# Performance work log

Measured on AMD Instinct MI355X. Metric: run time of the kernel, lower is better.

Reference implementation:

```python
import jax, jax.numpy as jnp
import numpy as np

T, B = 384, 128
IN_DIM, HID, OUT_DIM = 512, 1024, 512


def _lstm_step(h, c, x_t, Wx, Wh, b):
    # x_t: [B, D], h/c: [B, H]; gates order: i, f, g, o
    gates = x_t @ Wx + h @ Wh + b  # [B, 4H]
    i, f, g, o = jnp.split(gates, 4, axis=-1)
    c_new = jax.nn.sigmoid(f) * c + jax.nn.sigmoid(i) * jnp.tanh(g)
    h_new = jax.nn.sigmoid(o) * jnp.tanh(c_new)
    return h_new, c_new


def setup_inputs() -> dict:
    key = jax.random.key(0)
    ks = jax.random.split(key, 9)
    s_in = 1.0 / np.sqrt(IN_DIM)
    s_h = 1.0 / np.sqrt(HID)
    s_o = 1.0 / np.sqrt(OUT_DIM)
    return {
        "x": jax.random.normal(ks[0], (T, B, IN_DIM), dtype=jnp.float32),
        "hidden_state": jnp.zeros((1, B, HID), dtype=jnp.float32),
        "cell_state": jnp.zeros((1, B, HID), dtype=jnp.float32),
        "enc_Wx": jax.random.normal(ks[1], (IN_DIM, 4 * HID), dtype=jnp.float32) * s_in,
        "enc_Wh": jax.random.normal(ks[2], (HID, 4 * HID), dtype=jnp.float32) * s_h,
        "enc_b": jnp.zeros((4 * HID,), dtype=jnp.float32),
        "dec_Wx": jax.random.normal(ks[3], (OUT_DIM, 4 * HID), dtype=jnp.float32) * s_o,
        "dec_Wh": jax.random.normal(ks[4], (HID, 4 * HID), dtype=jnp.float32) * s_h,
        "dec_b": jnp.zeros((4 * HID,), dtype=jnp.float32),
        "fc_W": jax.random.normal(ks[5], (HID, OUT_DIM), dtype=jnp.float32) * s_h,
        "fc_b": jnp.zeros((OUT_DIM,), dtype=jnp.float32),
    }


def reference(x, hidden_state, cell_state, enc_Wx, enc_Wh, enc_b,
              dec_Wx, dec_Wh, dec_b, fc_W, fc_b):
    # ---- encoder: run LSTM over T steps, keep only final hidden state ----
    h0, c0 = hidden_state[0], cell_state[0]  # [B, H]

    def enc_step(carry, x_t):
        h, c = carry
        h, c = _lstm_step(h, c, x_t, enc_Wx, enc_Wh, enc_b)
        return (h, c), None

    (h_enc, _), _ = jax.lax.scan(enc_step, (h0, c0), x)

    y0 = jnp.zeros((B, OUT_DIM), dtype=x.dtype)
    c_dec0 = jnp.zeros((B, HID), dtype=x.dtype)

    def dec_step(carry, _):
        y, h, c = carry
        h, c = _lstm_step(h, c, y, dec_Wx, dec_Wh, dec_b)
        y = jax.nn.softmax(h @ fc_W + fc_b, axis=-1)  # softmax over dim=2
        return (y, h, c), y

    _, output = jax.lax.scan(dec_step, (y0, h_enc, c_dec0), None, length=T)
    return output  # [T, B, OUT_DIM]
```

## Files before the change

kernel.cpp:

```cpp
#include <hip/hip_runtime.h>


#define TS 384

typedef __attribute__((ext_vector_type(8))) short bf16x8;
typedef __attribute__((ext_vector_type(4))) float f32x4;

#define WS_XR 4096u
#define XR_SLOT 262144u
#define WS_HP (WS_XR + 4u*XR_SLOT)
#define HP_BUF 524288u
#define WS_FPN (WS_HP + 2u*HP_BUF)
#define WS_TOTAL (WS_FPN + 2097152u)

#define MFMA __builtin_amdgcn_mfma_f32_16x16x32_bf16

__device__ __forceinline__ unsigned short bf16r(float v) {
  unsigned u = __float_as_uint(v);
  u += 0x7FFFu + ((u >> 16) & 1u);
  return (unsigned short)(u >> 16);
}
__device__ __forceinline__ float bf2f(unsigned short h) {
  return __uint_as_float(((unsigned)h) << 16);
}
__device__ __forceinline__ void split2(float v, short& hi, short& lo) {
  unsigned short h = bf16r(v);
  float r = v - bf2f(h);
  hi = (short)h; lo = (short)bf16r(r);
}
__device__ __forceinline__ float sigm(float v)  { return 1.0f / (1.0f + __expf(-v)); }
__device__ __forceinline__ float tanhfa(float v){ return 1.0f - 2.0f / (__expf(2.0f*v) + 1.0f); }

__device__ __forceinline__ void st_u64(void* p, unsigned long long v) {
  __hip_atomic_store((unsigned long long*)p, v, __ATOMIC_RELAXED, __HIP_MEMORY_SCOPE_AGENT);
}
__device__ __forceinline__ unsigned long long ld_u64(const void* p) {
  return __hip_atomic_load((const unsigned long long*)p, __ATOMIC_RELAXED, __HIP_MEMORY_SCOPE_AGENT);
}
__device__ __forceinline__ void st_u32(unsigned* p, unsigned v) {
  __hip_atomic_store(p, v, __ATOMIC_RELAXED, __HIP_MEMORY_SCOPE_AGENT);
}
__device__ __forceinline__ unsigned ld_u32(const unsigned* p) {
  return __hip_atomic_load(p, __ATOMIC_RELAXED, __HIP_MEMORY_SCOPE_AGENT);
}
__device__ __forceinline__ void st_f32(float* p, float v) {
  __hip_atomic_store(p, v, __ATOMIC_RELAXED, __HIP_MEMORY_SCOPE_AGENT);
}
__device__ __forceinline__ float ld_f32(const float* p) {
  return __hip_atomic_load(p, __ATOMIC_RELAXED, __HIP_MEMORY_SCOPE_AGENT);
}

__device__ __forceinline__ void setflag(unsigned* flag, unsigned val) {
  asm volatile("s_waitcnt vmcnt(0)" ::: "memory");
  __syncthreads();
  if (threadIdx.x == 0)
    __hip_atomic_store(flag, val, __ATOMIC_RELAXED, __HIP_MEMORY_SCOPE_AGENT);
}
__device__ __forceinline__ void hwait(const unsigned* flags, unsigned* invdone_line,
                                      bool leader, unsigned target, int* sDead) {
  if (leader) {
    if (threadIdx.x < 64) {
      const unsigned long long* q = (const unsigned long long*)(flags + threadIdx.x * 4);
      unsigned spins = 0;
      for (;;) {
        unsigned long long q0 = ld_u64(q), q1 = ld_u64(q + 1);
        bool ok = ((unsigned)q0 >= target) && ((unsigned)(q0 >> 32) >= target)
               && ((unsigned)q1 >= target) && ((unsigned)(q1 >> 32) >= target);
        if (__all(ok)) break;
        if (++spins > (1u << 20)) { if (threadIdx.x == 0) *sDead = 1; break; }
      }
    }
    if (threadIdx.x == 0) {
      __builtin_amdgcn_fence(__ATOMIC_ACQUIRE, "agent");
      st_u32(invdone_line, target);
      asm volatile("s_waitcnt vmcnt(0)" ::: "memory");
    }
  } else {
    if (threadIdx.x == 0) {
      unsigned spins = 0;
      while (ld_u32(invdone_line) < target) {
        if (++spins > (1u << 20)) { *sDead = 1; break; }
      }
      asm volatile("buffer_inv sc0" ::: "memory");
      asm volatile("s_waitcnt vmcnt(0)" ::: "memory");
    }
  }
  __syncthreads();
}
__device__ __forceinline__ void wait128(const unsigned* flags, unsigned target, int* sDead) {
  if (threadIdx.x < 64) {
    const int i = threadIdx.x;
    const bool act = (i * 4) < 128;
    const unsigned long long* q = (const unsigned long long*)(flags + i * 4);
    unsigned spins = 0;
    for (;;) {
      bool ok = true;
      if (act) {
        unsigned long long q0 = ld_u64(q), q1 = ld_u64(q + 1);
        ok = ((unsigned)q0 >= target) && ((unsigned)(q0 >> 32) >= target)
          && ((unsigned)q1 >= target) && ((unsigned)(q1 >> 32) >= target);
      }
      if (__all(ok)) break;
      if (++spins > (1u << 20)) { if (i == 0) *sDead = 1; break; }
    }
  }
  __syncthreads();
}

__device__ void load_gate_weights(const float* __restrict__ Wx, const float* __restrict__ Wh,
                                  int p, short* sBh, short* sBl) {
  for (int idx = threadIdx.x; idx < 24576; idx += 1024) {
    int j = idx & 7, l = (idx >> 3) & 63, kb = idx >> 9;
    int k = kb * 32 + ((l >> 4) << 3) + j;
    int c = l & 15;
    int gcol = (c >> 2) * 1024 + p * 4 + (c & 3);
    float wv = (k < 512) ? Wx[(size_t)k * 4096 + gcol]
                         : Wh[(size_t)(k - 512) * 4096 + gcol];
    short hi, lo; split2(wv, hi, lo);
    sBh[idx] = hi; sBl[idx] = lo;
  }
}
__device__ void load_fc_weights(const float* __restrict__ fcW, int kg, int cg,
                                short* sFh, short* sFl) {
  for (int idx = threadIdx.x; idx < 4096; idx += 1024) {
    int j = idx & 7, l = (idx >> 3) & 63, kb = idx >> 9;
    int unit = kg * 256 + kb * 32 + ((l >> 4) << 3) + j;
    int col = cg * 16 + (l & 15);
    short hi, lo; split2(fcW[(size_t)unit * 512 + col], hi, lo);
    sFh[idx] = hi; sFl[idx] = lo;
  }
}

template<int NKB, int D>
__device__ __forceinline__ void gg_pipe(const short* AH_, const short* AL_,
    const short* BH_, const short* BL_, int mt, int l,
    int kbA0, int kbB0, f32x4* acc)
{
  const bf16x8* AH = (const bf16x8*)AH_;
  const bf16x8* AL = (const bf16x8*)AL_;
  const bf16x8* BH = (const bf16x8*)BH_;
  const bf16x8* BL = (const bf16x8*)BL_;
  bf16x8 pah[D], pal[D];
  #pragma unroll
  for (int i = 0; i < D; ++i) {
    pah[i] = AH[((kbA0 + i) * 8 + mt) * 64 + l];
    pal[i] = AL[((kbA0 + i) * 8 + mt) * 64 + l];
  }
  #pragma unroll
  for (int i = 0; i < NKB; ++i) {
    bf16x8 ah = pah[i % D], al = pal[i % D];
    if (i + D < NKB) {
      pah[i % D] = AH[((kbA0 + i + D) * 8 + mt) * 64 + l];
      pal[i % D] = AL[((kbA0 + i + D) * 8 + mt) * 64 + l];
    }
    bf16x8 bh = BH[(kbB0 + i) * 64 + l];
    bf16x8 bl = BL[(kbB0 + i) * 64 + l];
    const int a = (i & 1) * 3;
    acc[a + 0] = MFMA(ah, bh, acc[a + 0], 0, 0, 0);
    acc[a + 1] = MFMA(ah, bl, acc[a + 1], 0, 0, 0);
    acc[a + 2] = MFMA(al, bh, acc[a + 2], 0, 0, 0);
  }
}
__device__ __forceinline__ void gg_finish(f32x4* acc, int kh, int mt, int l,
                                          float* LDSgate) {
  f32x4 s = (acc[0] + acc[3]) + ((acc[1] + acc[4]) + (acc[2] + acc[5]));
  const int col = l & 15, r0 = mt * 16 + ((l >> 4) << 2);
  float* plane = LDSgate + kh * 2176;
  #pragma unroll
  for (int j = 0; j < 4; ++j) plane[(r0 + j) * 17 + col] = s[j];
}

__device__ __forceinline__ void conv_x(const float* __restrict__ xsrc,
                                       short* dstH, short* dstL, int p, int tl) {
  if (tl < 32) {
    int g = p * 32 + tl;
    int l = g & 63, mt = (g >> 6) & 7, kb = g >> 9;
    int row = mt * 16 + (l & 15), k = kb * 32 + ((l >> 4) << 3);
    const float* xs = xsrc + (size_t)row * 512 + k;
    unsigned long long h64[2] = {0, 0}, l64[2] = {0, 0};
    #pragma unroll
    for (int j = 0; j < 8; ++j) {
      short hi, lo; split2(xs[j], hi, lo);
      h64[j >> 2] |= (unsigned long long)(unsigned short)hi << ((j & 3) * 16);
      l64[j >> 2] |= (unsigned long long)(unsigned short)lo << ((j & 3) * 16);
    }
    int off = g * 8;
    st_u64(dstH + off, h64[0]); st_u64(dstH + off + 4, h64[1]);
    st_u64(dstL + off, l64[0]); st_u64(dstL + off + 4, l64[1]);
  }
}

__global__ void __launch_bounds__(1024, 1)
lstm12(const float* __restrict__ x, const float* __restrict__ h0p,
       const float* __restrict__ c0p, const float* __restrict__ eWx,
       const float* __restrict__ eWh, const float* __restrict__ eb,
       const float* __restrict__ dWx, const float* __restrict__ dWh,
       const float* __restrict__ db, const float* __restrict__ fcW,
       const float* __restrict__ fcb, float* __restrict__ out,
       char* __restrict__ ws)
{
  __shared__ __align__(16) short sBh[24576], sBl[24576];
  __shared__ __align__(16) short sFh[4096], sFl[4096];
  __shared__ float LDSgate[2 * 2176];
  __shared__ unsigned hsplit[512];
  __shared__ float ybuf[512];
  __shared__ float red[16];
  __shared__ int sDead, sLeader, sXcd;

  const int p = blockIdx.x, t = threadIdx.x;
  const int w = t >> 6, l = t & 63;
  const int mt = w & 7, kh = w >> 3;
  if (t == 0) sDead = 0;

  unsigned* hflag = (unsigned*)ws;
  unsigned* yflag = (unsigned*)(ws + 1024);
  unsigned* fflag = (unsigned*)(ws + 2048);
  unsigned* elect = (unsigned*)(ws + 3264);

  if (t == 0) {
    unsigned xcd;
    asm volatile("s_getreg_b32 %0, hwreg(HW_REG_XCC_ID)" : "=s"(xcd));
    xcd &= 7u;
    sXcd = (int)xcd;
    unsigned old = __hip_atomic_fetch_add(&elect[xcd], 1u, __ATOMIC_ACQ_REL,
                                          __HIP_MEMORY_SCOPE_AGENT);
    sLeader = (old == 0u) ? 1 : 0;
  }
  __syncthreads();
  const bool leader = (sLeader != 0);
  unsigned* invd = (unsigned*)(ws + 3328 + sXcd * 64);

  short* xrH[4]; short* xrL[4];
  #pragma unroll
  for (int s4 = 0; s4 < 4; ++s4) {
    xrH[s4] = (short*)(ws + WS_XR + s4 * XR_SLOT);
    xrL[s4] = (short*)(ws + WS_XR + s4 * XR_SLOT + 131072u);
  }
  short* hpH[2]; short* hpL[2];
  #pragma unroll
  for (int b2 = 0; b2 < 2; ++b2) {
    hpH[b2] = (short*)(ws + WS_HP + b2 * HP_BUF);
    hpL[b2] = (short*)(ws + WS_HP + b2 * HP_BUF + 262144u);
  }
  float* fp = (float*)(ws + WS_FPN);

  const int row_pw = t & 127, u_pw = (t >> 7) & 3;

  load_gate_weights(eWx, eWh, p, sBh, sBl);
  conv_x(x, xrH[0], xrL[0], p, t);
  conv_x(x + 65536, xrH[1], xrL[1], p, t);
  if (t < 64) {
    int hg = p * 64 + t;
    int ll = hg & 63, mtt = (hg >> 6) & 7, hk = hg >> 9;
    int row = mtt * 16 + (ll & 15), k = hk * 32 + ((ll >> 4) << 3);
    const float* hs = h0p + (size_t)row * 1024 + k;
    unsigned long long h64[2] = {0, 0}, l64[2] = {0, 0};
    #pragma unroll
    for (int j = 0; j < 8; ++j) {
      short hi, lo; split2(hs[j], hi, lo);
      h64[j >> 2] |= (unsigned long long)(unsigned short)hi << ((j & 3) * 16);
      l64[j >> 2] |= (unsigned long long)(unsigned short)lo << ((j & 3) * 16);
    }
    int off = hg * 8;
    st_u64(hpH[0] + off, h64[0]); st_u64(hpH[0] + off + 4, h64[1]);
    st_u64(hpL[0] + off, l64[0]); st_u64(hpL[0] + off + 4, l64[1]);
  }
  float creg = 0.f, bq0 = 0.f, bq1 = 0.f, bq2 = 0.f, bq3 = 0.f;
  if (t < 512) {
    creg = c0p[(size_t)row_pw * 1024 + p * 4 + u_pw];
    bq0 = eb[0 * 1024 + p * 4 + u_pw];
    bq1 = eb[1 * 1024 + p * 4 + u_pw];
    bq2 = eb[2 * 1024 + p * 4 + u_pw];
    bq3 = eb[3 * 1024 + p * 4 + u_pw];
  }
  setflag(&hflag[p], 1u);
  hwait(hflag, invd, leader, 1u, &sDead);
  if (sDead) return;

  for (int st = 0; st < TS; ++st) {
    int rb = st & 1, wb = rb ^ 1, xs = st & 3;
    f32x4 z = {0.f, 0.f, 0.f, 0.f};
    f32x4 acc[6] = {z, z, z, z, z, z};
    gg_pipe<8, 4>(xrH[xs], xrL[xs], sBh, sBl, mt, l, kh * 8, kh * 8, acc);
    hwait(hflag, invd, leader, (unsigned)(st + 1), &sDead);
    if (sDead) return;
    gg_pipe<16, 4>(hpH[rb], hpL[rb], sBh, sBl, mt, l, kh * 16, 16 + kh * 16, acc);
    gg_finish(acc, kh, mt, l, LDSgate);
    __syncthreads();
    if (t < 512) {
      float g0 = LDSgate[row_pw * 17 + 0  + u_pw] + LDSgate[2176 + row_pw * 17 + 0  + u_pw] + bq0;
      float g1 = LDSgate[row_pw * 17 + 4  + u_pw] + LDSgate[2176 + row_pw * 17 + 4  + u_pw] + bq1;
      float g2 = LDSgate[row_pw * 17 + 8  + u_pw] + LDSgate[2176 + row_pw * 17 + 8  + u_pw] + bq2;
      float g3 = LDSgate[row_pw * 17 + 12 + u_pw] + LDSgate[2176 + row_pw * 17 + 12 + u_pw] + bq3;
      creg = sigm(g1) * creg + sigm(g0) * tanhfa(g2);
      float h = sigm(g3) * tanhfa(creg);
      short hi, lo; split2(h, hi, lo);
      hsplit[u_pw * 128 + row_pw] = ((unsigned)(unsigned short)hi << 16) | (unsigned short)lo;
    } else if (st + 2 < TS) {
      conv_x(x + (size_t)(st + 2) * 65536, xrH[(st + 2) & 3], xrL[(st + 2) & 3], p, t - 512);
    }
    __syncthreads();
    if (t < 128) {
      int r = t;
      unsigned w0 = hsplit[r], w1 = hsplit[128 + r], w2 = hsplit[256 + r], w3 = hsplit[384 + r];
      unsigned long long hi64 = (unsigned long long)(w0 >> 16)
        | ((unsigned long long)(w1 >> 16) << 16)
        | ((unsigned long long)(w2 >> 16) << 32)
        | ((unsigned long long)(w3 >> 16) << 48);
      unsigned long long lo64 = (unsigned long long)(w0 & 0xFFFFu)
        | ((unsigned long long)(w1 & 0xFFFFu) << 16)
        | ((unsigned long long)(w2 & 0xFFFFu) << 32)
        | ((unsigned long long)(w3 & 0xFFFFu) << 48);
      int hk = p >> 3, mtt = r >> 4;
      int lane_ = (((p >> 1) & 3) << 4) | (r & 15);
      int off = ((hk * 8 + mtt) * 64 + lane_) * 8 + (p & 1) * 4;
      st_u64(hpH[wb] + off, hi64);
      st_u64(hpL[wb] + off, lo64);
    }
    setflag(&hflag[p], (unsigned)(st + 2));
  }

  load_gate_weights(dWx, dWh, p, sBh, sBl);
  if (p >= 128) load_fc_weights(fcW, (p - 128) >> 5, (p - 128) & 31, sFh, sFl);
  if (t < 32) {
    int off = (p * 32 + t) * 8;
    st_u64(xrH[0] + off, 0ull); st_u64(xrH[0] + off + 4, 0ull);
    st_u64(xrL[0] + off, 0ull); st_u64(xrL[0] + off + 4, 0ull);
  }
  creg = 0.0f;
  if (t < 512) {
    bq0 = db[0 * 1024 + p * 4 + u_pw];
    bq1 = db[1 * 1024 + p * 4 + u_pw];
    bq2 = db[2 * 1024 + p * 4 + u_pw];
    bq3 = db[3 * 1024 + p * 4 + u_pw];
  }
  float fcb_r = (t < 512) ? fcb[t] : 0.f;
  setflag(&hflag[p], (unsigned)(TS + 2));

  const unsigned DB = (unsigned)(TS + 2);
  for (int st = 0; st < TS; ++st) {
    const int rb = st & 1, wb = rb ^ 1;
    f32x4 z = {0.f, 0.f, 0.f, 0.f};
    f32x4 acc[6] = {z, z, z, z, z, z};
    hwait(hflag, invd, leader, DB + (unsigned)st, &sDead);
    if (sDead) return;
    if (p >= 128) {
      const int f = p - 128, kg = f >> 5, cg = f & 31;
      if (st >= 1) {
        const bf16x8* AH = (const bf16x8*)hpH[rb];
        const bf16x8* AL = (const bf16x8*)hpL[rb];
        const bf16x8* FB = (const bf16x8*)sFh;
        const bf16x8* FL = (const bf16x8*)sFl;
        f32x4 a0 = z, a1 = z, a2 = z;
        #pragma unroll
        for (int kb = 0; kb < 4; ++kb) {
          int gkb = kg * 8 + kh * 4 + kb;
          bf16x8 ah = AH[(gkb * 8 + mt) * 64 + l];
          bf16x8 al = AL[(gkb * 8 + mt) * 64 + l];
          bf16x8 bh = FB[(kh * 4 + kb) * 64 + l];
          bf16x8 bl = FL[(kh * 4 + kb) * 64 + l];
          a0 = MFMA(ah, bh, a0, 0, 0, 0);
          a1 = MFMA(ah, bl, a1, 0, 0, 0);
          a2 = MFMA(al, bh, a2, 0, 0, 0);
        }
        f32x4 s = a0 + (a1 + a2);
        int slice = kg * 2 + kh;
        int col = cg * 16 + (l & 15), r0 = mt * 16 + ((l >> 4) << 2);
        #pragma unroll
        for (int j = 0; j < 4; ++j)
          st_f32(&fp[(size_t)(slice * 128 + r0 + j) * 512 + col], s[j]);
        setflag(&fflag[f], (unsigned)st);
      }
      gg_pipe<16, 4>(hpH[rb], hpL[rb], sBh, sBl, mt, l, kh * 16, 16 + kh * 16, acc);
      if (st >= 1) { wait128(yflag, (unsigned)st, &sDead); if (sDead) return; }
      gg_pipe<8, 4>(xrH[rb], xrL[rb], sBh, sBl, mt, l, kh * 8, kh * 8, acc);
    } else {
      gg_pipe<16, 4>(hpH[rb], hpL[rb], sBh, sBl, mt, l, kh * 16, 16 + kh * 16, acc);
      if (st >= 1) {
        wait128(fflag, (unsigned)st, &sDead);
        if (sDead) return;
        float v = 0.f, e = 0.f, mx;
        if (t < 512) {
          float tv[8];
          #pragma unroll
          for (int s8 = 0; s8 < 8; ++s8)
            tv[s8] = ld_f32(&fp[(size_t)(s8 * 128 + p) * 512 + t]);
          v = fcb_r + ((tv[0] + tv[1]) + (tv[2] + tv[3]))
                    + ((tv[4] + tv[5]) + (tv[6] + tv[7]));
          mx = v;
          #pragma unroll
          for (int o = 32; o > 0; o >>= 1) mx = fmaxf(mx, __shfl_xor(mx, o));
          if (l == 0) red[w] = mx;
        }
        __syncthreads();
        if (t < 512) {
          mx = red[0];
          #pragma unroll
          for (int i = 1; i < 8; ++i) mx = fmaxf(mx, red[i]);
          e = __expf(v - mx);
          float ss = e;
          #pragma unroll
          for (int o = 32; o > 0; o >>= 1) ss += __shfl_xor(ss, o);
          if (l == 0) red[8 + w] = ss;
        }
        __syncthreads();
        if (t < 512) {
          float ss = (red[8] + red[9]) + (red[10] + red[11])
                   + (red[12] + red[13]) + (red[14] + red[15]);
          float y = e / ss;
          st_f32(&out[((size_t)(st - 1) * 128 + p) * 512 + t], y);
          ybuf[t] = y;
        }
        __syncthreads();
        if (t < 64) {
          int kb = t >> 2, seg = t & 3;
          int k = kb * 32 + seg * 8;
          int lane_ = (seg << 4) | (p & 15), mtt = p >> 4;
          int off = ((kb * 8 + mtt) * 64 + lane_) * 8;
          unsigned long long h64[2] = {0, 0}, l64[2] = {0, 0};
          #pragma unroll
          for (int j = 0; j < 8; ++j) {
            short hi, lo; split2(ybuf[k + j], hi, lo);
            h64[j >> 2] |= (unsigned long long)(unsigned short)hi << ((j & 3) * 16);
            l64[j >> 2] |= (unsigned long long)(unsigned short)lo << ((j & 3) * 16);
          }
          st_u64(xrH[rb] + off, h64[0]); st_u64(xrH[rb] + off + 4, h64[1]);
          st_u64(xrL[rb] + off, l64[0]); st_u64(xrL[rb] + off + 4, l64[1]);
        }
        setflag(&yflag[p], (unsigned)st);
        wait128(yflag, (unsigned)st, &sDead);
        if (sDead) return;
      }
      gg_pipe<8, 4>(xrH[rb], xrL[rb], sBh, sBl, mt, l, kh * 8, kh * 8, acc);
    }
    gg_finish(acc, kh, mt, l, LDSgate);
    __syncthreads();
    if (t < 512) {
      float g0 = LDSgate[row_pw * 17 + 0  + u_pw] + LDSgate[2176 + row_pw * 17 + 0  + u_pw] + bq0;
      float g1 = LDSgate[row_pw * 17 + 4  + u_pw] + LDSgate[2176 + row_pw * 17 + 4  + u_pw] + bq1;
      float g2 = LDSgate[row_pw * 17 + 8  + u_pw] + LDSgate[2176 + row_pw * 17 + 8  + u_pw] + bq2;
      float g3 = LDSgate[row_pw * 17 + 12 + u_pw] + LDSgate[2176 + row_pw * 17 + 12 + u_pw] + bq3;
      creg = sigm(g1) * creg + sigm(g0) * tanhfa(g2);
      float h = sigm(g3) * tanhfa(creg);
      short hi, lo; split2(h, hi, lo);
      hsplit[u_pw * 128 + row_pw] = ((unsigned)(unsigned short)hi << 16) | (unsigned short)lo;
    }
    __syncthreads();
    if (t < 128) {
      int r = t;
      unsigned w0 = hsplit[r], w1 = hsplit[128 + r], w2 = hsplit[256 + r], w3 = hsplit[384 + r];
      unsigned long long hi64 = (unsigned long long)(w0 >> 16)
        | ((unsigned long long)(w1 >> 16) << 16)
        | ((unsigned long long)(w2 >> 16) << 32)
        | ((unsigned long long)(w3 >> 16) << 48);
      unsigned long long lo64 = (unsigned long long)(w0 & 0xFFFFu)
        | ((unsigned long long)(w1 & 0xFFFFu) << 16)
        | ((unsigned long long)(w2 & 0xFFFFu) << 32)
        | ((unsigned long long)(w3 & 0xFFFFu) << 48);
      int hk = p >> 3, mtt = r >> 4;
      int lane_ = (((p >> 1) & 3) << 4) | (r & 15);
      int off = ((hk * 8 + mtt) * 64 + lane_) * 8 + (p & 1) * 4;
      st_u64(hpH[wb] + off, hi64);
      st_u64(hpL[wb] + off, lo64);
    }
    setflag(&hflag[p], DB + (unsigned)(st + 1));
  }

  {
    const int rb = TS & 1;
    hwait(hflag, invd, leader, DB + (unsigned)TS, &sDead);
    if (sDead) return;
    if (p >= 128) {
      const int f = p - 128, kg = f >> 5, cg = f & 31;
      const bf16x8* AH = (const bf16x8*)hpH[rb];
      const bf16x8* AL = (const bf16x8*)hpL[rb];
      const bf16x8* FB = (const bf16x8*)sFh;
      const bf16x8* FL = (const bf16x8*)sFl;
      f32x4 z = {0.f, 0.f, 0.f, 0.f};
      f32x4 a0 = z, a1 = z, a2 = z;
      #pragma unroll
      for (int kb = 0; kb < 4; ++kb) {
        int gkb = kg * 8 + kh * 4 + kb;
        bf16x8 ah = AH[(gkb * 8 + mt) * 64 + l];
        bf16x8 al = AL[(gkb * 8 + mt) * 64 + l];
        bf16x8 bh = FB[(kh * 4 + kb) * 64 + l];
        bf16x8 bl = FL[(kh * 4 + kb) * 64 + l];
        a0 = MFMA(ah, bh, a0, 0, 0, 0);
        a1 = MFMA(ah, bl, a1, 0, 0, 0);
        a2 = MFMA(al, bh, a2, 0, 0, 0);
      }
      f32x4 s = a0 + (a1 + a2);
      int slice = kg * 2 + kh;
      int col = cg * 16 + (l & 15), r0 = mt * 16 + ((l >> 4) << 2);
      #pragma unroll
      for (int j = 0; j < 4; ++j)
        st_f32(&fp[(size_t)(slice * 128 + r0 + j) * 512 + col], s[j]);
      setflag(&fflag[f], (unsigned)TS);
    } else {
      wait128(fflag, (unsigned)TS, &sDead);
      if (sDead) return;
      float v = 0.f, e = 0.f, mx;
      if (t < 512) {
        float tv[8];
        #pragma unroll
        for (int s8 = 0; s8 < 8; ++s8)
          tv[s8] = ld_f32(&fp[(size_t)(s8 * 128 + p) * 512 + t]);
        v = fcb_r + ((tv[0] + tv[1]) + (tv[2] + tv[3]))
                  + ((tv[4] + tv[5]) + (tv[6] + tv[7]));
        mx = v;
        #pragma unroll
        for (int o = 32; o > 0; o >>= 1) mx = fmaxf(mx, __shfl_xor(mx, o));
        if (l == 0) red[w] = mx;
      }
      __syncthreads();
      if (t < 512) {
        mx = red[0];
        #pragma unroll
        for (int i = 1; i < 8; ++i) mx = fmaxf(mx, red[i]);
        e = __expf(v - mx);
        float ss = e;
        #pragma unroll
        for (int o = 32; o > 0; o >>= 1) ss += __shfl_xor(ss, o);
        if (l == 0) red[8 + w] = ss;
      }
      __syncthreads();
      if (t < 512) {
        float ss = (red[8] + red[9]) + (red[10] + red[11])
                 + (red[12] + red[13]) + (red[14] + red[15]);
        st_f32(&out[((size_t)(TS - 1) * 128 + p) * 512 + t], e / ss);
      }
    }
  }
}

extern "C" void kernel_launch(void* const* d_in, const int* in_sizes, int n_in,
                              void* d_out, int out_size, void* d_ws, size_t ws_size,
                              hipStream_t stream) {
  const float* x   = (const float*)d_in[0];
  const float* h0  = (const float*)d_in[1];
  const float* c0  = (const float*)d_in[2];
  const float* eWx = (const float*)d_in[3];
  const float* eWh = (const float*)d_in[4];
  const float* eb  = (const float*)d_in[5];
  const float* dWx = (const float*)d_in[6];
  const float* dWh = (const float*)d_in[7];
  const float* db  = (const float*)d_in[8];
  const float* fcW = (const float*)d_in[9];
  const float* fcb = (const float*)d_in[10];
  float* out = (float*)d_out;

  if (ws_size < (size_t)WS_TOTAL) {
    hipMemsetAsync(d_out, 0xFF, (size_t)out_size * sizeof(float), stream);
    return;
  }
  hipMemsetAsync(d_ws, 0, 4096, stream);
  hipLaunchKernelGGL(lstm12, dim3(256), dim3(1024), 0, stream,
                     x, h0, c0, eWx, eWh, eb, dWx, dWh, db, fcW, fcb, out,
                     (char*)d_ws);
}
```

Measured before the change: 13.74 ms.

## Use cached stores for h/x staging with a cross-XCD writeback barrier

```diff
diff --git a/kernel.cpp b/kernel.cpp
--- a/kernel.cpp
+++ b/kernel.cpp
@@ -31,23 +31,26 @@
 __device__ __forceinline__ float sigm(float v)  { return 1.0f / (1.0f + __expf(-v)); }
 __device__ __forceinline__ float tanhfa(float v){ return 1.0f - 2.0f / (__expf(2.0f*v) + 1.0f); }
 
-__device__ __forceinline__ void st_u64(void* p, unsigned long long v) {
+__device__ __forceinline__ void st_u64_uc(void* p, unsigned long long v) {
   __hip_atomic_store((unsigned long long*)p, v, __ATOMIC_RELAXED, __HIP_MEMORY_SCOPE_AGENT);
 }
-__device__ __forceinline__ unsigned long long ld_u64(const void* p) {
+__device__ __forceinline__ unsigned long long ld_u64_uc(const void* p) {
   return __hip_atomic_load((const unsigned long long*)p, __ATOMIC_RELAXED, __HIP_MEMORY_SCOPE_AGENT);
 }
-__device__ __forceinline__ void st_u32(unsigned* p, unsigned v) {
+__device__ __forceinline__ void st_u32_uc(unsigned* p, unsigned v) {
   __hip_atomic_store(p, v, __ATOMIC_RELAXED, __HIP_MEMORY_SCOPE_AGENT);
 }
-__device__ __forceinline__ unsigned ld_u32(const unsigned* p) {
+__device__ __forceinline__ unsigned ld_u32_uc(const unsigned* p) {
   return __hip_atomic_load(p, __ATOMIC_RELAXED, __HIP_MEMORY_SCOPE_AGENT);
 }
-__device__ __forceinline__ void st_f32(float* p, float v) {
+__device__ __forceinline__ void st_f32_uc(float* p, float v) {
   __hip_atomic_store(p, v, __ATOMIC_RELAXED, __HIP_MEMORY_SCOPE_AGENT);
 }
-__device__ __forceinline__ float ld_f32(const float* p) {
+__device__ __forceinline__ float ld_f32_uc(const float* p) {
   return __hip_atomic_load(p, __ATOMIC_RELAXED, __HIP_MEMORY_SCOPE_AGENT);
+}
+__device__ __forceinline__ void st_u64_c(void* p, unsigned long long v) {
+  *(volatile unsigned long long*)p = v;
 }
 
 __device__ __forceinline__ void setflag(unsigned* flag, unsigned val) {
@@ -56,14 +59,15 @@
   if (threadIdx.x == 0)
     __hip_atomic_store(flag, val, __ATOMIC_RELAXED, __HIP_MEMORY_SCOPE_AGENT);
 }
-__device__ __forceinline__ void hwait(const unsigned* flags, unsigned* invdone_line,
-                                      bool leader, unsigned target, int* sDead) {
+__device__ __forceinline__ void hwait(const unsigned* flags, unsigned* wbdone,
+                                      unsigned* invdone_line, bool leader,
+                                      unsigned target, int* sDead) {
   if (leader) {
     if (threadIdx.x < 64) {
       const unsigned long long* q = (const unsigned long long*)(flags + threadIdx.x * 4);
       unsigned spins = 0;
       for (;;) {
-        unsigned long long q0 = ld_u64(q), q1 = ld_u64(q + 1);
+        unsigned long long q0 = ld_u64_uc(q), q1 = ld_u64_uc(q + 1);
         bool ok = ((unsigned)q0 >= target) && ((unsigned)(q0 >> 32) >= target)
                && ((unsigned)q1 >= target) && ((unsigned)(q1 >> 32) >= target);
         if (__all(ok)) break;
@@ -71,41 +75,17 @@
       }
     }
     if (threadIdx.x == 0) {
-      __builtin_amdgcn_fence(__ATOMIC_ACQUIRE, "agent");
-      st_u32(invdone_line, target);
+      __builtin_amdgcn_fence(__ATOMIC_RELEASE, "agent");
       asm volatile("s_waitcnt vmcnt(0)" ::: "memory");
-    }
-  } else {
-    if (threadIdx.x == 0) {
-      unsigned spins = 0;
-      while (ld_u32(invdone_line) < target) {
-        if (++spins > (1u << 20)) { *sDead = 1; break; }
-      }
-      asm volatile("buffer_inv sc0" ::: "memory");
-      asm volatile("s_waitcnt vmcnt(0)" ::: "memory");
+      st_u32_uc(wbdone + (int)( ((size_t)invdone_line >> 6) & 7 ), 0);
     }
   }
   __syncthreads();
-}
-__device__ __forceinline__ void wait128(const unsigned* flags, unsigned target, int* sDead) {
-  if (threadIdx.x < 64) {
-    const int i = threadIdx.x;
-    const bool act = (i * 4) < 128;
-    const unsigned long long* q = (const unsigned long long*)(flags + i * 4);
-    unsigned spins = 0;
-    for (;;) {
-      bool ok = true;
-      if (act) {
-        unsigned long long q0 = ld_u64(q), q1 = ld_u64(q + 1);
-        ok = ((unsigned)q0 >= target) && ((unsigned)(q0 >> 32) >= target)
-          && ((unsigned)q1 >= target) && ((unsigned)(q1 >> 32) >= target);
-      }
-      if (__all(ok)) break;
-      if (++spins > (1u << 20)) { if (i == 0) *sDead = 1; break; }
-    }
-  }
-  __syncthreads();
-}
+  (void)wbdone;
+  (void)invdone_line;
+  (void)sDead;
+}
+
 
 __device__ void load_gate_weights(const float* __restrict__ Wx, const float* __restrict__ Wh,
                                   int p, short* sBh, short* sBl) {
@@ -185,13 +165,13 @@
       l64[j >> 2] |= (unsigned long long)(unsigned short)lo << ((j & 3) * 16);
     }
     int off = g * 8;
-    st_u64(dstH + off, h64[0]); st_u64(dstH + off + 4, h64[1]);
-    st_u64(dstL + off, l64[0]); st_u64(dstL + off + 4, l64[1]);
+    st_u64_c(dstH + off, h64[0]); st_u64_c(dstH + off + 4, h64[1]);
+    st_u64_c(dstL + off, l64[0]); st_u64_c(dstL + off + 4, l64[1]);
   }
 }
 
 __global__ void __launch_bounds__(1024, 1)
-lstm12(const float* __restrict__ x, const float* __restrict__ h0p,
+lstm13(const float* __restrict__ x, const float* __restrict__ h0p,
        const float* __restrict__ c0p, const float* __restrict__ eWx,
        const float* __restrict__ eWh, const float* __restrict__ eb,
        const float* __restrict__ dWx, const float* __restrict__ dWh,
@@ -212,10 +192,11 @@
   const int mt = w & 7, kh = w >> 3;
   if (t == 0) sDead = 0;
 
-  unsigned* hflag = (unsigned*)ws;
-  unsigned* yflag = (unsigned*)(ws + 1024);
-  unsigned* fflag = (unsigned*)(ws + 2048);
-  unsigned* elect = (unsigned*)(ws + 3264);
+  unsigned* hflag  = (unsigned*)ws;
+  unsigned* yflag  = (unsigned*)(ws + 1024);
+  unsigned* fflag  = (unsigned*)(ws + 2048);
+  unsigned* elect  = (unsigned*)(ws + 3264);
+  unsigned* wbdone = (unsigned*)(ws + 3904);
 
   if (t == 0) {
     unsigned xcd;
@@ -228,7 +209,71 @@
   }
   __syncthreads();
   const bool leader = (sLeader != 0);
-  unsigned* invd = (unsigned*)(ws + 3328 + sXcd * 64);
+  const int myxcd = sXcd;
+  unsigned* invd = (unsigned*)(ws + 3328 + myxcd * 64);
+
+  auto HWAIT = [&](unsigned target) {
+    if (leader) {
+      if (t < 64) {
+        const unsigned long long* q = (const unsigned long long*)(hflag + t * 4);
+        unsigned spins = 0;
+        for (;;) {
+          unsigned long long q0 = ld_u64_uc(q), q1 = ld_u64_uc(q + 1);
+          bool ok = ((unsigned)q0 >= target) && ((unsigned)(q0 >> 32) >= target)
+                 && ((unsigned)q1 >= target) && ((unsigned)(q1 >> 32) >= target);
+          if (__all(ok)) break;
+          if (++spins > (1u << 20)) { if (t == 0) sDead = 1; break; }
+        }
+      }
+      if (t == 0) {
+        __builtin_amdgcn_fence(__ATOMIC_RELEASE, "agent");
+        asm volatile("s_waitcnt vmcnt(0)" ::: "memory");
+        st_u32_uc(&wbdone[myxcd], target);
+        unsigned spins = 0;
+        for (;;) {
+          unsigned long long a = ld_u64_uc(wbdone), b = ld_u64_uc(wbdone + 2);
+          unsigned long long c = ld_u64_uc(wbdone + 4), d = ld_u64_uc(wbdone + 6);
+          bool ok = ((unsigned)a >= target) && ((unsigned)(a >> 32) >= target)
+                 && ((unsigned)b >= target) && ((unsigned)(b >> 32) >= target)
+                 && ((unsigned)c >= target) && ((unsigned)(c >> 32) >= target)
+                 && ((unsigned)d >= target) && ((unsigned)(d >> 32) >= target);
+          if (ok) break;
+          if (++spins > (1u << 20)) { sDead = 1; break; }
+        }
+        __builtin_amdgcn_fence(__ATOMIC_ACQUIRE, "agent");
+        st_u32_uc(invd, target);
+        asm volatile("s_waitcnt vmcnt(0)" ::: "memory");
+      }
+    } else {
+      if (t == 0) {
+        unsigned spins = 0;
+        while (ld_u32_uc(invd) < target) {
+          if (++spins > (1u << 20)) { sDead = 1; break; }
+        }
+        asm volatile("buffer_inv sc0" ::: "memory");
+        asm volatile("s_waitcnt vmcnt(0)" ::: "memory");
+      }
+    }
+    __syncthreads();
+  };
+  auto WAIT128 = [&](const unsigned* flags, unsigned target) {
+    if (t < 64) {
+      const bool act = (t * 4) < 128;
+      const unsigned long long* q = (const unsigned long long*)(flags + t * 4);
+      unsigned spins = 0;
+      for (;;) {
+        bool ok = true;
+        if (act) {
+          unsigned long long q0 = ld_u64_uc(q), q1 = ld_u64_uc(q + 1);
+          ok = ((unsigned)q0 >= target) && ((unsigned)(q0 >> 32) >= target)
+            && ((unsigned)q1 >= target) && ((unsigned)(q1 >> 32) >= target);
+        }
+        if (__all(ok)) break;
+        if (++spins > (1u << 20)) { if (t == 0) sDead = 1; break; }
+      }
+    }
+    __syncthreads();
+  };
 
   short* xrH[4]; short* xrL[4];
   #pragma unroll
@@ -262,8 +307,8 @@
       l64[j >> 2] |= (unsigned long long)(unsigned short)lo << ((j & 3) * 16);
     }
     int off = hg * 8;
-    st_u64(hpH[0] + off, h64[0]); st_u64(hpH[0] + off + 4, h64[1]);
-    st_u64(hpL[0] + off, l64[0]); st_u64(hpL[0] + off + 4, l64[1]);
+    st_u64_c(hpH[0] + off, h64[0]); st_u64_c(hpH[0] + off + 4, h64[1]);
+    st_u64_c(hpL[0] + off, l64[0]); st_u64_c(hpL[0] + off + 4, l64[1]);
   }
   float creg = 0.f, bq0 = 0.f, bq1 = 0.f, bq2 = 0.f, bq3 = 0.f;
   if (t < 512) {
@@ -274,7 +319,7 @@
     bq3 = eb[3 * 1024 + p * 4 + u_pw];
   }
   setflag(&hflag[p], 1u);
-  hwait(hflag, invd, leader, 1u, &sDead);
+  HWAIT(1u);
   if (sDead) return;
 
   for (int st = 0; st < TS; ++st) {
@@ -282,7 +327,7 @@
     f32x4 z = {0.f, 0.f, 0.f, 0.f};
     f32x4 acc[6] = {z, z, z, z, z, z};
     gg_pipe<8, 4>(xrH[xs], xrL[xs], sBh, sBl, mt, l, kh * 8, kh * 8, acc);
-    hwait(hflag, invd, leader, (unsigned)(st + 1), &sDead);
+    HWAIT((unsigned)(st + 1));
     if (sDead) return;
     gg_pipe<16, 4>(hpH[rb], hpL[rb], sBh, sBl, mt, l, kh * 16, 16 + kh * 16, acc);
     gg_finish(acc, kh, mt, l, LDSgate);
@@ -314,8 +359,8 @@
       int hk = p >> 3, mtt = r >> 4;
       int lane_ = (((p >> 1) & 3) << 4) | (r & 15);
       int off = ((hk * 8 + mtt) * 64 + lane_) * 8 + (p & 1) * 4;
-      st_u64(hpH[wb] + off, hi64);
-      st_u64(hpL[wb] + off, lo64);
+      st_u64_c(hpH[wb] + off, hi64);
+      st_u64_c(hpL[wb] + off, lo64);
     }
     setflag(&hflag[p], (unsigned)(st + 2));
   }
@@ -324,8 +369,8 @@
   if (p >= 128) load_fc_weights(fcW, (p - 128) >> 5, (p - 128) & 31, sFh, sFl);
   if (t < 32) {
     int off = (p * 32 + t) * 8;
-    st_u64(xrH[0] + off, 0ull); st_u64(xrH[0] + off + 4, 0ull);
-    st_u64(xrL[0] + off, 0ull); st_u64(xrL[0] + off + 4, 0ull);
+    st_u64_c(xrH[0] + off, 0ull); st_u64_c(xrH[0] + off + 4, 0ull);
+    st_u64_c(xrL[0] + off, 0ull); st_u64_c(xrL[0] + off + 4, 0ull);
   }
   creg = 0.0f;
   if (t < 512) {
@@ -342,7 +387,7 @@
     const int rb = st & 1, wb = rb ^ 1;
     f32x4 z = {0.f, 0.f, 0.f, 0.f};
     f32x4 acc[6] = {z, z, z, z, z, z};
-    hwait(hflag, invd, leader, DB + (unsigned)st, &sDead);
+    HWAIT(DB + (unsigned)st);
     if (sDead) return;
     if (p >= 128) {
       const int f = p - 128, kg = f >> 5, cg = f & 31;
@@ -368,23 +413,23 @@
         int col = cg * 16 + (l & 15), r0 = mt * 16 + ((l >> 4) << 2);
         #pragma unroll
         for (int j = 0; j < 4; ++j)
-          st_f32(&fp[(size_t)(slice * 128 + r0 + j) * 512 + col], s[j]);
+          st_f32_uc(&fp[(size_t)(slice * 128 + r0 + j) * 512 + col], s[j]);
         setflag(&fflag[f], (unsigned)st);
       }
       gg_pipe<16, 4>(hpH[rb], hpL[rb], sBh, sBl, mt, l, kh * 16, 16 + kh * 16, acc);
-      if (st >= 1) { wait128(yflag, (unsigned)st, &sDead); if (sDead) return; }
+      if (st >= 1) { WAIT128(yflag, (unsigned)st); if (sDead) return; }
       gg_pipe<8, 4>(xrH[rb], xrL[rb], sBh, sBl, mt, l, kh * 8, kh * 8, acc);
     } else {
       gg_pipe<16, 4>(hpH[rb], hpL[rb], sBh, sBl, mt, l, kh * 16, 16 + kh * 16, acc);
       if (st >= 1) {
-        wait128(fflag, (unsigned)st, &sDead);
+        WAIT128(fflag, (unsigned)st);
         if (sDead) return;
         float v = 0.f, e = 0.f, mx;
         if (t < 512) {
           float tv[8];
           #pragma unroll
           for (int s8 = 0; s8 < 8; ++s8)
-            tv[s8] = ld_f32(&fp[(size_t)(s8 * 128 + p) * 512 + t]);
+            tv[s8] = ld_f32_uc(&fp[(size_t)(s8 * 128 + p) * 512 + t]);
           v = fcb_r + ((tv[0] + tv[1]) + (tv[2] + tv[3]))
                     + ((tv[4] + tv[5]) + (tv[6] + tv[7]));
           mx = v;
@@ -408,7 +453,7 @@
           float ss = (red[8] + red[9]) + (red[10] + red[11])
                    + (red[12] + red[13]) + (red[14] + red[15]);
           float y = e / ss;
-          st_f32(&out[((size_t)(st - 1) * 128 + p) * 512 + t], y);
+          st_f32_uc(&out[((size_t)(st - 1) * 128 + p) * 512 + t], y);
           ybuf[t] = y;
         }
         __syncthreads();
@@ -424,11 +469,11 @@
             h64[j >> 2] |= (unsigned long long)(unsigned short)hi << ((j & 3) * 16);
             l64[j >> 2] |= (unsigned long long)(unsigned short)lo << ((j & 3) * 16);
           }
-          st_u64(xrH[rb] + off, h64[0]); st_u64(xrH[rb] + off + 4, h64[1]);
-          st_u64(xrL[rb] + off, l64[0]); st_u64(xrL[rb] + off + 4, l64[1]);
+          st_u64_uc(xrH[rb] + off, h64[0]); st_u64_uc(xrH[rb] + off + 4, h64[1]);
+          st_u64_uc(xrL[rb] + off, l64[0]); st_u64_uc(xrL[rb] + off + 4, l64[1]);
         }
         setflag(&yflag[p], (unsigned)st);
-        wait128(yflag, (unsigned)st, &sDead);
+        WAIT128(yflag, (unsigned)st);
         if (sDead) return;
       }
       gg_pipe<8, 4>(xrH[rb], xrL[rb], sBh, sBl, mt, l, kh * 8, kh * 8, acc);
@@ -460,15 +505,15 @@
       int hk = p >> 3, mtt = r >> 4;
       int lane_ = (((p >> 1) & 3) << 4) | (r & 15);
       int off = ((hk * 8 + mtt) * 64 + lane_) * 8 + (p & 1) * 4;
-      st_u64(hpH[wb] + off, hi64);
-      st_u64(hpL[wb] + off, lo64);
+      st_u64_c(hpH[wb] + off, hi64);
+      st_u64_c(hpL[wb] + off, lo64);
     }
     setflag(&hflag[p], DB + (unsigned)(st + 1));
   }
 
   {
     const int rb = TS & 1;
-    hwait(hflag, invd, leader, DB + (unsigned)TS, &sDead);
+    HWAIT(DB + (unsigned)TS);
     if (sDead) return;
     if (p >= 128) {
       const int f = p - 128, kg = f >> 5, cg = f & 31;
@@ -494,17 +539,17 @@
       int col = cg * 16 + (l & 15), r0 = mt * 16 + ((l >> 4) << 2);
       #pragma unroll
       for (int j = 0; j < 4; ++j)
-        st_f32(&fp[(size_t)(slice * 128 + r0 + j) * 512 + col], s[j]);
-      setflag(&fflag[f], (unsigned)TS);
+        st_f32_uc(&fp[(size_t)(slice * 128 + r0 + j) * 512 + col], s[j]);
+      setflag(&fflag[p - 128], (unsigned)TS);
     } else {
-      wait128(fflag, (unsigned)TS, &sDead);
+      WAIT128(fflag, (unsigned)TS);
       if (sDead) return;
       float v = 0.f, e = 0.f, mx;
       if (t < 512) {
         float tv[8];
         #pragma unroll
         for (int s8 = 0; s8 < 8; ++s8)
-          tv[s8] = ld_f32(&fp[(size_t)(s8 * 128 + p) * 512 + t]);
+          tv[s8] = ld_f32_uc(&fp[(size_t)(s8 * 128 + p) * 512 + t]);
         v = fcb_r + ((tv[0] + tv[1]) + (tv[2] + tv[3]))
                   + ((tv[4] + tv[5]) + (tv[6] + tv[7]));
         mx = v;
@@ -527,7 +572,7 @@
       if (t < 512) {
         float ss = (red[8] + red[9]) + (red[10] + red[11])
                  + (red[12] + red[13]) + (red[14] + red[15]);
-        st_f32(&out[((size_t)(TS - 1) * 128 + p) * 512 + t], e / ss);
+        st_f32_uc(&out[((size_t)(TS - 1) * 128 + p) * 512 + t], e / ss);
       }
     }
   }
@@ -554,7 +599,7 @@
     return;
   }
   hipMemsetAsync(d_ws, 0, 4096, stream);
-  hipLaunchKernelGGL(lstm12, dim3(256), dim3(1024), 0, stream,
+  hipLaunchKernelGGL(lstm13, dim3(256), dim3(1024), 0, stream,
                      x, h0, c0, eWx, eWh, eb, dWx, dWh, db, fcW, fcb, out,
                      (char*)d_ws);
 }
```

After: 14.65 ms. +6.7%, slower.

## Read x directly in fp32 per step and warm h buffer into cache

Applied to the files above, without the earlier changes.

```diff
diff --git a/kernel.cpp b/kernel.cpp
--- a/kernel.cpp
+++ b/kernel.cpp
@@ -161,6 +161,32 @@
     acc[a + 2] = MFMA(al, bh, acc[a + 2], 0, 0, 0);
   }
 }
+__device__ __forceinline__ void gg_x_direct(const float* __restrict__ xsrc,
+    const short* BH_, const short* BL_, int mt, int kh, int l, f32x4* acc)
+{
+  const bf16x8* BH = (const bf16x8*)BH_;
+  const bf16x8* BL = (const bf16x8*)BL_;
+  const int row = mt * 16 + (l & 15);
+  const int kbase = kh * 256 + ((l >> 4) << 3);
+  #pragma unroll
+  for (int kb = 0; kb < 8; ++kb) {
+    const float* xp = xsrc + (size_t)row * 512 + kbase + kb * 32;
+    float4 f0 = *(const float4*)xp;
+    float4 f1 = *(const float4*)(xp + 4);
+    union { bf16x8 v; short s[8]; } Ah, Al;
+    split2(f0.x, Ah.s[0], Al.s[0]); split2(f0.y, Ah.s[1], Al.s[1]);
+    split2(f0.z, Ah.s[2], Al.s[2]); split2(f0.w, Ah.s[3], Al.s[3]);
+    split2(f1.x, Ah.s[4], Al.s[4]); split2(f1.y, Ah.s[5], Al.s[5]);
+    split2(f1.z, Ah.s[6], Al.s[6]); split2(f1.w, Ah.s[7], Al.s[7]);
+    const int kbl = kh * 8 + kb;
+    bf16x8 bh = BH[kbl * 64 + l];
+    bf16x8 bl = BL[kbl * 64 + l];
+    const int a = (kb & 1) * 3;
+    acc[a + 0] = MFMA(Ah.v, bh, acc[a + 0], 0, 0, 0);
+    acc[a + 1] = MFMA(Ah.v, bl, acc[a + 1], 0, 0, 0);
+    acc[a + 2] = MFMA(Al.v, bh, acc[a + 2], 0, 0, 0);
+  }
+}
 __device__ __forceinline__ void gg_finish(f32x4* acc, int kh, int mt, int l,
                                           float* LDSgate) {
   f32x4 s = (acc[0] + acc[3]) + ((acc[1] + acc[4]) + (acc[2] + acc[5]));
@@ -169,29 +195,20 @@
   #pragma unroll
   for (int j = 0; j < 4; ++j) plane[(r0 + j) * 17 + col] = s[j];
 }
-
-__device__ __forceinline__ void conv_x(const float* __restrict__ xsrc,
-                                       short* dstH, short* dstL, int p, int tl) {
-  if (tl < 32) {
-    int g = p * 32 + tl;
-    int l = g & 63, mt = (g >> 6) & 7, kb = g >> 9;
-    int row = mt * 16 + (l & 15), k = kb * 32 + ((l >> 4) << 3);
-    const float* xs = xsrc + (size_t)row * 512 + k;
-    unsigned long long h64[2] = {0, 0}, l64[2] = {0, 0};
-    #pragma unroll
-    for (int j = 0; j < 8; ++j) {
-      short hi, lo; split2(xs[j], hi, lo);
-      h64[j >> 2] |= (unsigned long long)(unsigned short)hi << ((j & 3) * 16);
-      l64[j >> 2] |= (unsigned long long)(unsigned short)lo << ((j & 3) * 16);
-    }
-    int off = g * 8;
-    st_u64(dstH + off, h64[0]); st_u64(dstH + off + 4, h64[1]);
-    st_u64(dstL + off, l64[0]); st_u64(dstL + off + 4, l64[1]);
-  }
+__device__ __forceinline__ void warm_h(const short* hH, const short* hL, int t) {
+  const unsigned* wH = (const unsigned*)hH;
+  const unsigned* wL = (const unsigned*)hL;
+  unsigned d = 0;
+  #pragma unroll
+  for (int i = 0; i < 4; ++i) {
+    d += wH[(t + i * 1024) * 16];
+    d += wL[(t + i * 1024) * 16];
+  }
+  asm volatile("" :: "v"(d));
 }
 
 __global__ void __launch_bounds__(1024, 1)
-lstm12(const float* __restrict__ x, const float* __restrict__ h0p,
+lstm14(const float* __restrict__ x, const float* __restrict__ h0p,
        const float* __restrict__ c0p, const float* __restrict__ eWx,
        const float* __restrict__ eWh, const float* __restrict__ eb,
        const float* __restrict__ dWx, const float* __restrict__ dWh,
@@ -230,9 +247,9 @@
   const bool leader = (sLeader != 0);
   unsigned* invd = (unsigned*)(ws + 3328 + sXcd * 64);
 
-  short* xrH[4]; short* xrL[4];
-  #pragma unroll
-  for (int s4 = 0; s4 < 4; ++s4) {
+  short* xrH[2]; short* xrL[2];
+  #pragma unroll
+  for (int s4 = 0; s4 < 2; ++s4) {
     xrH[s4] = (short*)(ws + WS_XR + s4 * XR_SLOT);
     xrL[s4] = (short*)(ws + WS_XR + s4 * XR_SLOT + 131072u);
   }
@@ -247,8 +264,6 @@
   const int row_pw = t & 127, u_pw = (t >> 7) & 3;
 
   load_gate_weights(eWx, eWh, p, sBh, sBl);
-  conv_x(x, xrH[0], xrL[0], p, t);
-  conv_x(x + 65536, xrH[1], xrL[1], p, t);
   if (t < 64) {
     int hg = p * 64 + t;
     int ll = hg & 63, mtt = (hg >> 6) & 7, hk = hg >> 9;
@@ -278,12 +293,13 @@
   if (sDead) return;
 
   for (int st = 0; st < TS; ++st) {
-    int rb = st & 1, wb = rb ^ 1, xs = st & 3;
+    int rb = st & 1, wb = rb ^ 1;
     f32x4 z = {0.f, 0.f, 0.f, 0.f};
     f32x4 acc[6] = {z, z, z, z, z, z};
-    gg_pipe<8, 4>(xrH[xs], xrL[xs], sBh, sBl, mt, l, kh * 8, kh * 8, acc);
+    gg_x_direct(x + (size_t)st * 65536, sBh, sBl, mt, kh, l, acc);
     hwait(hflag, invd, leader, (unsigned)(st + 1), &sDead);
     if (sDead) return;
+    warm_h(hpH[rb], hpL[rb], t);
     gg_pipe<16, 4>(hpH[rb], hpL[rb], sBh, sBl, mt, l, kh * 16, 16 + kh * 16, acc);
     gg_finish(acc, kh, mt, l, LDSgate);
     __syncthreads();
@@ -296,8 +312,6 @@
       float h = sigm(g3) * tanhfa(creg);
       short hi, lo; split2(h, hi, lo);
       hsplit[u_pw * 128 + row_pw] = ((unsigned)(unsigned short)hi << 16) | (unsigned short)lo;
-    } else if (st + 2 < TS) {
-      conv_x(x + (size_t)(st + 2) * 65536, xrH[(st + 2) & 3], xrL[(st + 2) & 3], p, t - 512);
     }
     __syncthreads();
     if (t < 128) {
@@ -344,6 +358,7 @@
     f32x4 acc[6] = {z, z, z, z, z, z};
     hwait(hflag, invd, leader, DB + (unsigned)st, &sDead);
     if (sDead) return;
+    warm_h(hpH[rb], hpL[rb], t);
     if (p >= 128) {
       const int f = p - 128, kg = f >> 5, cg = f & 31;
       if (st >= 1) {
@@ -554,7 +569,7 @@
     return;
   }
   hipMemsetAsync(d_ws, 0, 4096, stream);
-  hipLaunchKernelGGL(lstm12, dim3(256), dim3(1024), 0, stream,
+  hipLaunchKernelGGL(lstm14, dim3(256), dim3(1024), 0, stream,
                      x, h0, c0, eWx, eWh, eb, dWx, dWh, db, fcW, fcb, out,
                      (char*)d_ws);
 }
```

Result: slower. 17.97 ms (+30.9%).
